# Kernel tuning notes

Hardware: AMD Instinct MI355X
Metric: run time of the kernel (lower is better)

Reference implementation:

```python
import jax, jax.numpy as jnp
import numpy as np

H_DIM = 768
N_HEADS = 12
HEAD_DIM = H_DIM // N_HEADS  # 64
LOW_RANK = 2
LR_DIM = H_DIM // LOW_RANK   # 384
SEQ = 2048
WINDOW = 1024
EOT = 50256


def _rope_tables(seq_len, dim):
    pos = jnp.arange(seq_len, dtype=jnp.float32)[:, None]
    div = jnp.exp(jnp.arange(0, dim, 2, dtype=jnp.float32) * (-np.log(10000.0) / dim))
    emb = pos * div  # (S, dim/2)
    sin = jnp.concatenate([jnp.sin(emb), jnp.sin(emb)], axis=-1)  # (S, dim)
    cos = jnp.concatenate([jnp.cos(emb), jnp.cos(emb)], axis=-1)
    return sin, cos


def _apply_rope(x, sin, cos):
    # x: (B, H, S, d); sin/cos: (S, d)
    half = x.shape[-1] // 2
    rot = jnp.concatenate([-x[..., half:], x[..., :half]], axis=-1)
    return x * cos + rot * sin


def setup_inputs() -> dict:
    key = jax.random.key(0)
    ks = jax.random.split(key, 20)
    x = jax.random.normal(ks[0], (1, SEQ, H_DIM), dtype=jnp.float32)
    # tokens with document boundaries every ~512 tokens
    tok = jax.random.randint(ks[1], (SEQ,), 0, 50257)
    tok = tok.at[::512].set(EOT)

    def lin(k, fan_in, fan_out):
        w = jax.random.normal(k, (fan_in, fan_out), dtype=jnp.float32) * 0.02
        b = jnp.zeros((fan_out,), dtype=jnp.float32)
        return w, b

    qd_w, qd_b = lin(ks[2], H_DIM, LR_DIM)
    qu_w, qu_b = lin(ks[3], LR_DIM, H_DIM)
    qr_w, qr_b = lin(ks[4], H_DIM, HEAD_DIM)
    kvd_w, kvd_b = lin(ks[5], H_DIM, LR_DIM)
    ku_w, ku_b = lin(ks[6], LR_DIM, H_DIM)
    vu_w, vu_b = lin(ks[7], LR_DIM, H_DIM * 2)
    kr_w, kr_b = lin(ks[8], H_DIM, HEAD_DIM)
    o_w, o_b = lin(ks[9], H_DIM * 2, H_DIM)
    return dict(x=x, token_seq=tok,
                qd_w=qd_w, qd_b=qd_b, qu_w=qu_w, qu_b=qu_b,
                qr_w=qr_w, qr_b=qr_b, kvd_w=kvd_w, kvd_b=kvd_b,
                ku_w=ku_w, ku_b=ku_b, vu_w=vu_w, vu_b=vu_b,
                kr_w=kr_w, kr_b=kr_b, o_w=o_w, o_b=o_b)


def _mla_forward(x, token_seq, qd_w, qd_b, qu_w, qu_b, qr_w, qr_b,
                 kvd_w, kvd_b, ku_w, ku_b, vu_w, vu_b, kr_w, kr_b, o_w, o_b):
    B, S, _ = x.shape
    sin, cos = _rope_tables(S, HEAD_DIM)
    scale = (2 * HEAD_DIM) ** (-0.5)

    # queries: low-rank down/up + shared rotary part
    q = (x @ qd_w + qd_b) @ qu_w + qu_b                     # (B,S,H_DIM)
    q = q.reshape(B, S, N_HEADS, HEAD_DIM).transpose(0, 2, 1, 3)
    qr = (x @ qr_w + qr_b)[:, None, :, :]                   # (B,1,S,hd)
    qr = jnp.broadcast_to(qr, (B, N_HEADS, S, HEAD_DIM))
    qr = _apply_rope(qr, sin, cos)
    q = jnp.concatenate([q, qr], axis=-1)                   # (B,nh,S,2hd)

    # shared low-rank kv latent
    lkv = x @ kvd_w + kvd_b                                 # (B,S,LR)
    k = (lkv @ ku_w + ku_b).reshape(B, S, N_HEADS, HEAD_DIM).transpose(0, 2, 1, 3)
    kr = (x @ kr_w + kr_b)[:, None, :, :]
    kr = jnp.broadcast_to(kr, (B, N_HEADS, S, HEAD_DIM))
    kr = _apply_rope(kr, sin, cos)
    k = jnp.concatenate([k, kr], axis=-1)                   # (B,nh,S,2hd)

    v = (lkv @ vu_w + vu_b).reshape(B, S, N_HEADS, 2 * HEAD_DIM).transpose(0, 2, 1, 3)

    # mask: causal & same-document & sliding window (<1024)
    docs = jnp.cumsum(token_seq == EOT)
    qi = jnp.arange(S)
    mask = (qi[:, None] >= qi[None, :]) \
           & (docs[:, None] == docs[None, :]) \
           & (qi[:, None] - qi[None, :] < WINDOW)           # (S,S)

    scores = jnp.einsum('bhqd,bhkd->bhqk', q, k) * scale
    scores = jnp.where(mask, scores, -jnp.inf)
    attn = jax.nn.softmax(scores, axis=-1)
    out = jnp.einsum('bhqk,bhkd->bhqd', attn, v)            # (B,nh,S,2hd)
    out = out.transpose(0, 2, 1, 3).reshape(B, S, 2 * H_DIM)
    return out @ o_w + o_b


def reference(x, token_seq, qd_w, qd_b, qu_w, qu_b, qr_w, qr_b,
              kvd_w, kvd_b, ku_w, ku_b, vu_w, vu_b, kr_w, kr_b, o_w, o_b):
    return _mla_forward(x, token_seq, qd_w, qd_b, qu_w, qu_b, qr_w, qr_b,
                        kvd_w, kvd_b, ku_w, ku_b, vu_w, vu_b, kr_w, kr_b, o_w, o_b)
```

## Files before the change

kernel.cpp:

```cpp
#include <hip/hip_runtime.h>
#include <hip/hip_bf16.h>
#include <math.h>

#define SEQ 2048
#define HDIM 768
#define NH 12
#define HD 64
#define LR 384
#define EOT 50256

typedef short s16x8 __attribute__((ext_vector_type(8)));
typedef float f32x4 __attribute__((ext_vector_type(4)));
typedef unsigned short u16x8 __attribute__((ext_vector_type(8)));
typedef unsigned short u16x4 __attribute__((ext_vector_type(4)));

__device__ __forceinline__ unsigned short f2bf(float f) {
    union { float f; unsigned u; } v; v.f = f;
    unsigned r = v.u + 0x7fffu + ((v.u >> 16) & 1u);
    return (unsigned short)(r >> 16);
}

__device__ __forceinline__ void gl_lds16(const void* g, void* l) {
    __builtin_amdgcn_global_load_lds(
        (const __attribute__((address_space(1))) unsigned int*)g,
        (__attribute__((address_space(3))) unsigned int*)l, 16, 0, 0);
}

__global__ __launch_bounds__(256)
void transpose_pack_all(const float* w0, const float* w1, const float* w2, const float* w3,
                        const float* w4, const float* w5, const float* w6, const float* w7,
                        unsigned short* t0, unsigned short* t1, unsigned short* t2, unsigned short* t3,
                        unsigned short* t4, unsigned short* t5, unsigned short* t6, unsigned short* t7,
                        const float* x, unsigned short* xb,
                        const float* qd_b, const float* kvd_b, const float* qr_b, const float* kr_b,
                        const float* qu_b, const float* ku_b, const float* vu_b,
                        float* biasA, float* biasB,
                        const int* tok, int* lastEOT) {
    __shared__ float t[64][65];
    __shared__ int smax[256];
    int b = blockIdx.x;
    const int tid = threadIdx.x;
    if (b == 1129) {
        const int base = tid * 8;
        int v[8];
        int mx = 0;
#pragma unroll
        for (int j = 0; j < 8; ++j) {
            int i = base + j;
            int f = (tok[i] == EOT) ? i : 0;
            mx = max(mx, f);
            v[j] = mx;
        }
        smax[tid] = mx;
        __syncthreads();
        for (int off = 1; off < 256; off <<= 1) {
            int val = (tid >= off) ? smax[tid - off] : 0;
            __syncthreads();
            smax[tid] = max(smax[tid], val);
            __syncthreads();
        }
        int pre = (tid > 0) ? smax[tid - 1] : 0;
#pragma unroll
        for (int j = 0; j < 8; ++j) lastEOT[base + j] = max(pre, v[j]);
        return;
    }
    if (b == 1128) {
        for (int i = tid; i < 896; i += 256) {
            float v;
            if (i < 384) v = qd_b[i];
            else if (i < 768) v = kvd_b[i - 384];
            else if (i < 832) v = qr_b[i - 768];
            else v = kr_b[i - 832];
            biasA[i] = v;
        }
        for (int i = tid; i < 3072; i += 256) {
            float v;
            if (i < 768) v = qu_b[i];
            else if (i < 1536) v = ku_b[i - 768];
            else v = vu_b[i - 1536];
            biasB[i] = v;
        }
        return;
    }
    if (b >= 744) {
        int b2 = b - 744;
        int row0 = (b2 / 12) * 64, col0 = (b2 % 12) * 64;
#pragma unroll
        for (int i = 0; i < 16; ++i) {
            int idx = tid + i * 256;
            int r = idx >> 6, c = idx & 63;
            xb[(size_t)(row0 + r) * HDIM + col0 + c] = f2bf(x[(size_t)(row0 + r) * HDIM + col0 + c]);
        }
        return;
    }
    const float* W; unsigned short* T; int K, N, lt;
    if      (b < 72)  { W = w0; T = t0; K = 768;  N = 384;  lt = b; }
    else if (b < 144) { W = w1; T = t1; K = 384;  N = 768;  lt = b - 72; }
    else if (b < 156) { W = w2; T = t2; K = 768;  N = 64;   lt = b - 144; }
    else if (b < 228) { W = w3; T = t3; K = 768;  N = 384;  lt = b - 156; }
    else if (b < 300) { W = w4; T = t4; K = 384;  N = 768;  lt = b - 228; }
    else if (b < 444) { W = w5; T = t5; K = 384;  N = 1536; lt = b - 300; }
    else if (b < 456) { W = w6; T = t6; K = 768;  N = 64;   lt = b - 444; }
    else              { W = w7; T = t7; K = 1536; N = 768;  lt = b - 456; }
    const int tn = N >> 6;
    const int n0 = (lt % tn) * 64, k0 = (lt / tn) * 64;
#pragma unroll
    for (int i = 0; i < 16; ++i) {
        int idx = tid + i * 256;
        int k = idx >> 6, n = idx & 63;
        t[k][n] = W[(size_t)(k0 + k) * N + n0 + n];
    }
    __syncthreads();
#pragma unroll
    for (int i = 0; i < 16; ++i) {
        int idx = tid + i * 256;
        int n = idx >> 6, k = idx & 63;
        T[(size_t)(n0 + n) * K + k0 + k] = f2bf(t[k][n]);
    }
}

template <int FUSE>
__global__ __launch_bounds__(256)
void gemm_mfma_kernel(const unsigned short* __restrict__ A, const unsigned short* __restrict__ Bt,
                      const float* __restrict__ bias,
                      void* __restrict__ O0, void* __restrict__ O1, void* __restrict__ O2,
                      int K, int lda) {
    __shared__ unsigned short As[2][128 * 64];
    __shared__ unsigned short Bs[2][64 * 64];
    const int tid = threadIdx.x;
    const int w = tid >> 6, lane = tid & 63, lr = lane & 15, lg = lane >> 4;
    const int row0 = blockIdx.y * 128, col0 = blockIdx.x * 64;
    const int wr = (w >> 1) * 64, wc = (w & 1) * 32;
    const unsigned short* Ab = A + ((FUSE == 2 && col0 >= 768) ? 384 : 0);

    f32x4 acc[4][2];
#pragma unroll
    for (int i = 0; i < 4; ++i)
#pragma unroll
        for (int j = 0; j < 2; ++j) acc[i][j] = f32x4{0.f, 0.f, 0.f, 0.f};

    auto stage = [&](int buf, int kt) {
#pragma unroll
        for (int i = 0; i < 4; ++i) {
            int c = tid + i * 256;
            int row = c >> 3, dgL = c & 7;
            gl_lds16(Ab + (size_t)(row0 + row) * lda + kt + (dgL ^ (row & 7)) * 8, &As[buf][c * 8]);
        }
#pragma unroll
        for (int i = 0; i < 2; ++i) {
            int c = tid + i * 256;
            int n = c >> 3, dgL = c & 7;
            gl_lds16(Bt + (size_t)(col0 + n) * K + kt + (dgL ^ (n & 7)) * 8, &Bs[buf][c * 8]);
        }
    };

    const int nkt = K >> 6;
    stage(0, 0);
    for (int t = 0; t < nkt; ++t) {
        __syncthreads();
        if (t + 1 < nkt) stage((t + 1) & 1, (t + 1) << 6);
        const unsigned short* asb = As[t & 1];
        const unsigned short* bsb = Bs[t & 1];
#pragma unroll
        for (int kk = 0; kk < 2; ++kk) {
            const int kbyte = kk * 64 + lg * 16;
#pragma unroll
            for (int mi = 0; mi < 4; ++mi) {
                const int row = wr + mi * 16 + lr;
                s16x8 a = *(const s16x8*)&asb[row * 64 + ((kbyte ^ ((row & 7) << 4)) >> 1)];
#pragma unroll
                for (int ni = 0; ni < 2; ++ni) {
                    const int n = wc + ni * 16 + lr;
                    s16x8 bfr = *(const s16x8*)&bsb[n * 64 + ((kbyte ^ ((n & 7) << 4)) >> 1)];
                    acc[mi][ni] = __builtin_amdgcn_mfma_f32_16x16x32_bf16(a, bfr, acc[mi][ni], 0, 0, 0);
                }
            }
        }
    }

    if (FUSE == 1 && col0 >= 768) {
        __syncthreads();
        float* rt = (float*)&As[0][0];
#pragma unroll
        for (int mi = 0; mi < 4; ++mi)
#pragma unroll
            for (int ni = 0; ni < 2; ++ni) {
                const int cl = wc + ni * 16 + lr;
                const float bv = bias[col0 + cl];
#pragma unroll
                for (int j = 0; j < 4; ++j)
                    rt[(wr + mi * 16 + lg * 4 + j) * 64 + cl] = acc[mi][ni][j] + bv;
            }
        __syncthreads();
        unsigned short* dst = (col0 == 768) ? (unsigned short*)O1 : (unsigned short*)O2;
        const int row = tid >> 1;
        const int i0 = (tid & 1) * 16;
        const float srow = (float)(row0 + row);
#pragma unroll
        for (int ii = 0; ii < 16; ++ii) {
            const int i = i0 + ii;
            float a = rt[row * 64 + i], b = rt[row * 64 + 32 + i];
            float div = expf((float)(2 * i) * (-logf(10000.0f) / 64.0f));
            float emb = srow * div;
            float sn, cs;
            __sincosf(emb, &sn, &cs);
            dst[(size_t)(row0 + row) * 64 + i]      = f2bf(a * cs - b * sn);
            dst[(size_t)(row0 + row) * 64 + 32 + i] = f2bf(b * cs + a * sn);
        }
        return;
    }

#pragma unroll
    for (int mi = 0; mi < 4; ++mi) {
#pragma unroll
        for (int ni = 0; ni < 2; ++ni) {
            const int col = col0 + wc + ni * 16 + lr;
            const float bv = bias[col];
            const int rbase = row0 + wr + mi * 16 + lg * 4;
            if (FUSE == 0) {
#pragma unroll
                for (int j = 0; j < 4; ++j)
                    ((float*)O0)[(size_t)(rbase + j) * HDIM + col] = acc[mi][ni][j] + bv;
            } else if (FUSE == 1) {
#pragma unroll
                for (int j = 0; j < 4; ++j)
                    ((unsigned short*)O0)[(size_t)(rbase + j) * HDIM + col] = f2bf(acc[mi][ni][j] + bv);
            } else {
                if (col < 768) {
                    const int hh = col >> 6, d = col & 63;
#pragma unroll
                    for (int j = 0; j < 4; ++j)
                        ((unsigned short*)O0)[(size_t)(rbase + j) * (NH * 64) + hh * 64 + d] = f2bf(acc[mi][ni][j] + bv);
                } else if (col < 1536) {
                    const int c2 = col - 768;
                    const int hh = c2 >> 6, d = c2 & 63;
#pragma unroll
                    for (int j = 0; j < 4; ++j)
                        ((unsigned short*)O1)[(size_t)(rbase + j) * (NH * 64) + hh * 64 + d] = f2bf(acc[mi][ni][j] + bv);
                } else {
                    const int c2 = col - 1536;
                    const int hh = c2 >> 7, d = c2 & 127;
                    u16x4 pk;
#pragma unroll
                    for (int j = 0; j < 4; ++j) pk[j] = f2bf(acc[mi][ni][j] + bv);
                    *(u16x4*)((unsigned short*)O2 + (size_t)(hh * 128 + d) * SEQ + rbase) = pk;
                }
            }
        }
    }
}

__global__ __launch_bounds__(256)
void attn_mfma_kernel(const unsigned short* __restrict__ qbuf,
                      const unsigned short* __restrict__ qrb,
                      const unsigned short* __restrict__ kbuf,
                      const unsigned short* __restrict__ krb,
                      const unsigned short* __restrict__ vbT,
                      const int* __restrict__ lastEOT,
                      unsigned short* __restrict__ aob) {
    __shared__ unsigned short Ks[2][64 * 128];
    __shared__ unsigned short Vt[2][128 * 64];
    __shared__ unsigned short Pa[4][16 * 64];

    const int h    = blockIdx.y;
    const int q0   = blockIdx.x * 64;
    const int tid  = threadIdx.x;
    const int w    = tid >> 6;
    const int lane = tid & 63;
    const int lr   = lane & 15;
    const int lg   = lane >> 4;

    const int qrow0 = q0 + w * 16 + lg * 4;
    const int qminw = q0 + w * 16;
    const int qmaxw = qminw + 15;
    const int leMinW = lastEOT[qminw];
    const int leMaxW = lastEOT[qmaxw];
    int rs[4];
#pragma unroll
    for (int r = 0; r < 4; ++r) rs[r] = lastEOT[qrow0 + r];

    s16x8 aq[4];
    {
        const int s = q0 + w * 16 + lr;
        const unsigned short* qp = qbuf + ((size_t)s * NH + h) * 64 + lg * 8;
        aq[0] = *(const s16x8*)qp;
        aq[1] = *(const s16x8*)(qp + 32);
        const unsigned short* qrp = qrb + (size_t)s * 64 + lg * 8;
        aq[2] = *(const s16x8*)qrp;
        aq[3] = *(const s16x8*)(qrp + 32);
    }

    const int kt0 = lastEOT[q0] & ~63;
    const int ntiles = (q0 + 64 - kt0) >> 6;

    float lsum[4] = {0.f, 0.f, 0.f, 0.f};
    f32x4 o[8];
#pragma unroll
    for (int n = 0; n < 8; ++n) o[n] = f32x4{0.f, 0.f, 0.f, 0.f};

    const float scale = 0.088388347648318447f;

    auto stage = [&](int buf, int k0) {
#pragma unroll
        for (int i = 0; i < 4; ++i) {
            const int c = tid + i * 256;
            const int key = c >> 4, dgL = c & 15;
            const int dg = dgL ^ (key & 7);
            const unsigned short* src = (dg < 8)
                ? kbuf + ((size_t)(k0 + key) * NH + h) * 64 + dg * 8
                : krb + (size_t)(k0 + key) * 64 + (dg - 8) * 8;
            gl_lds16(src, &Ks[buf][c * 8]);
        }
#pragma unroll
        for (int i = 0; i < 4; ++i) {
            const int c = tid + i * 256;
            const int dim = c >> 3, kgL = c & 7;
            gl_lds16(vbT + ((size_t)h * 128 + dim) * SEQ + k0 + (kgL ^ (dim & 7)) * 8, &Vt[buf][c * 8]);
        }
    };

    stage(0, kt0);
    for (int t = 0; t < ntiles; ++t) {
        const int k0 = kt0 + t * 64;
        __syncthreads();
        if (t + 1 < ntiles) stage((t + 1) & 1, k0 + 64);

        if (k0 > qmaxw || k0 + 63 < leMinW) continue;

        const unsigned short* ksb = Ks[t & 1];
        const unsigned short* vtb = Vt[t & 1];

        f32x4 s[4];
#pragma unroll
        for (int n = 0; n < 4; ++n) s[n] = f32x4{0.f, 0.f, 0.f, 0.f};
#pragma unroll
        for (int n = 0; n < 4; ++n) {
            const int key = n * 16 + lr;
            const int swz = (key & 7) << 4;
#pragma unroll
            for (int kk = 0; kk < 4; ++kk) {
                const int colb = (kk * 64 + lg * 16) ^ swz;
                s16x8 bk = *(const s16x8*)&ksb[key * 128 + (colb >> 1)];
                s[n] = __builtin_amdgcn_mfma_f32_16x16x32_bf16(aq[kk], bk, s[n], 0, 0, 0);
            }
        }

        const bool full = (k0 + 63 <= qminw) && (k0 >= leMaxW);
        float p[4][4];
        if (full) {
#pragma unroll
            for (int n = 0; n < 4; ++n)
#pragma unroll
                for (int r = 0; r < 4; ++r) {
                    float pv = __expf(s[n][r] * scale);
                    p[n][r] = pv;
                    lsum[r] += pv;
                }
        } else {
#pragma unroll
            for (int n = 0; n < 4; ++n) {
                const int k = k0 + n * 16 + lr;
#pragma unroll
                for (int r = 0; r < 4; ++r) {
                    const int qq = qrow0 + r;
                    const bool valid = (k <= qq) && (k >= rs[r]);
                    float pv = valid ? __expf(s[n][r] * scale) : 0.f;
                    p[n][r] = pv;
                    lsum[r] += pv;
                }
            }
        }

#pragma unroll
        for (int n = 0; n < 4; ++n)
#pragma unroll
            for (int r = 0; r < 4; ++r) {
                const int ql = lg * 4 + r;
                const int key = n * 16 + lr;
                const int byteoff = (key * 2) ^ ((ql & 7) << 4);
                Pa[w][ql * 64 + (byteoff >> 1)] = f2bf(p[n][r]);
            }

#pragma unroll
        for (int kk2 = 0; kk2 < 2; ++kk2) {
            const int keyb = kk2 * 32 + lg * 8;
            s16x8 ap = *(const s16x8*)&Pa[w][lr * 64 + ((((keyb * 2) ^ ((lr & 7) << 4))) >> 1)];
#pragma unroll
            for (int n = 0; n < 8; ++n) {
                const int dim = n * 16 + lr;
                s16x8 bv = *(const s16x8*)&vtb[dim * 64 + ((((keyb * 2) ^ ((dim & 7) << 4))) >> 1)];
                o[n] = __builtin_amdgcn_mfma_f32_16x16x32_bf16(ap, bv, o[n], 0, 0, 0);
            }
        }
    }

#pragma unroll
    for (int off = 1; off < 16; off <<= 1)
#pragma unroll
        for (int r = 0; r < 4; ++r) lsum[r] += __shfl_xor(lsum[r], off);

    float inv[4];
#pragma unroll
    for (int r = 0; r < 4; ++r) inv[r] = 1.f / lsum[r];
#pragma unroll
    for (int n = 0; n < 8; ++n)
#pragma unroll
        for (int r = 0; r < 4; ++r) {
            const int qq = qrow0 + r;
            aob[(size_t)qq * (2 * HDIM) + h * 128 + n * 16 + lr] = f2bf(o[n][r] * inv[r]);
        }
}

extern "C" void kernel_launch(void* const* d_in, const int* in_sizes, int n_in,
                              void* d_out, int out_size, void* d_ws, size_t ws_size,
                              hipStream_t stream) {
    (void)in_sizes; (void)n_in; (void)out_size; (void)ws_size;
    const float* x     = (const float*)d_in[0];
    const int*   tok   = (const int*)d_in[1];
    const float* qd_w  = (const float*)d_in[2];
    const float* qd_b  = (const float*)d_in[3];
    const float* qu_w  = (const float*)d_in[4];
    const float* qu_b  = (const float*)d_in[5];
    const float* qr_w  = (const float*)d_in[6];
    const float* qr_b  = (const float*)d_in[7];
    const float* kvd_w = (const float*)d_in[8];
    const float* kvd_b = (const float*)d_in[9];
    const float* ku_w  = (const float*)d_in[10];
    const float* ku_b  = (const float*)d_in[11];
    const float* vu_w  = (const float*)d_in[12];
    const float* vu_b  = (const float*)d_in[13];
    const float* kr_w  = (const float*)d_in[14];
    const float* kr_b  = (const float*)d_in[15];
    const float* o_w   = (const float*)d_in[16];
    const float* o_b   = (const float*)d_in[17];
    float* out = (float*)d_out;

    unsigned short* ws = (unsigned short*)d_ws;
    unsigned short* xb   = ws;
    unsigned short* lqkv = xb   + (size_t)SEQ * HDIM;
    unsigned short* qbuf = lqkv + (size_t)SEQ * HDIM;
    unsigned short* kbuf = qbuf + (size_t)SEQ * NH * 64;
    unsigned short* qrb  = kbuf + (size_t)SEQ * NH * 64;
    unsigned short* krb  = qrb  + (size_t)SEQ * 64;
    unsigned short* vbT  = krb  + (size_t)SEQ * 64;
    unsigned short* aob  = vbT  + (size_t)NH * 128 * SEQ;
    unsigned short* B1   = aob  + (size_t)SEQ * 2 * HDIM;
    unsigned short* B2   = B1   + (size_t)896 * HDIM;
    unsigned short* to   = B2   + (size_t)3072 * LR;
    float* biasA = (float*)(to + (size_t)HDIM * 2 * HDIM);
    float* biasB = biasA + 896;
    int* lastEOT = (int*)(biasB + 3072);

    unsigned short* tqd  = B1;
    unsigned short* tkvd = B1 + (size_t)384 * 768;
    unsigned short* tqr  = B1 + (size_t)768 * 768;
    unsigned short* tkr  = B1 + (size_t)832 * 768;
    unsigned short* tqu  = B2;
    unsigned short* tku  = B2 + (size_t)768 * 384;
    unsigned short* tvu  = B2 + (size_t)1536 * 384;

    transpose_pack_all<<<1130, 256, 0, stream>>>(qd_w, qu_w, qr_w, kvd_w, ku_w, vu_w, kr_w, o_w,
                                                 tqd, tqu, tqr, tkvd, tku, tvu, tkr, to,
                                                 x, xb, qd_b, kvd_b, qr_b, kr_b, qu_b, ku_b, vu_b,
                                                 biasA, biasB, tok, lastEOT);

    gemm_mfma_kernel<1><<<dim3(14, 16), 256, 0, stream>>>(xb, B1, biasA, lqkv, qrb, krb, HDIM, HDIM);
    gemm_mfma_kernel<2><<<dim3(48, 16), 256, 0, stream>>>(lqkv, B2, biasB, qbuf, kbuf, vbT, LR, HDIM);

    attn_mfma_kernel<<<dim3(SEQ / 64, NH), 256, 0, stream>>>(qbuf, qrb, kbuf, krb, vbT, lastEOT, aob);

    gemm_mfma_kernel<0><<<dim3(12, 16), 256, 0, stream>>>(aob, to, o_b, out, nullptr, nullptr, 2 * HDIM, 2 * HDIM);
}
```

Baseline: 81.75 us.

## Load K/V fragments directly from global memory instead of LDS staging

Drops the double-buffered LDS staging of K and V tiles and the per-tile block barrier. Each wave now reads its K/Kr and transposed-V MFMA operands straight from global memory and loops only over its own key range, set by its first row's document start. The aim is to remove barrier stalls and the work of tiles a wave skips. In exchange, the four waves each fetch the same K/V data, so global/L2 traffic rises and there is no software prefetch to hide load latency.

```diff
diff --git a/kernel.cpp b/kernel.cpp
--- a/kernel.cpp
+++ b/kernel.cpp
@@ -258,8 +258,6 @@
                       const unsigned short* __restrict__ vbT,
                       const int* __restrict__ lastEOT,
                       unsigned short* __restrict__ aob) {
-    __shared__ unsigned short Ks[2][64 * 128];
-    __shared__ unsigned short Vt[2][128 * 64];
     __shared__ unsigned short Pa[4][16 * 64];
 
     const int h    = blockIdx.y;
@@ -290,8 +288,8 @@
         aq[3] = *(const s16x8*)(qrp + 32);
     }
 
-    const int kt0 = lastEOT[q0] & ~63;
-    const int ntiles = (q0 + 64 - kt0) >> 6;
+    const int kt0 = leMinW & ~63;
+    const int ntiles = (qmaxw >> 6) - (kt0 >> 6) + 1;
 
     float lsum[4] = {0.f, 0.f, 0.f, 0.f};
     f32x4 o[8];
@@ -300,49 +298,24 @@
 
     const float scale = 0.088388347648318447f;
 
-    auto stage = [&](int buf, int k0) {
-#pragma unroll
-        for (int i = 0; i < 4; ++i) {
-            const int c = tid + i * 256;
-            const int key = c >> 4, dgL = c & 15;
-            const int dg = dgL ^ (key & 7);
-            const unsigned short* src = (dg < 8)
-                ? kbuf + ((size_t)(k0 + key) * NH + h) * 64 + dg * 8
-                : krb + (size_t)(k0 + key) * 64 + (dg - 8) * 8;
-            gl_lds16(src, &Ks[buf][c * 8]);
-        }
-#pragma unroll
-        for (int i = 0; i < 4; ++i) {
-            const int c = tid + i * 256;
-            const int dim = c >> 3, kgL = c & 7;
-            gl_lds16(vbT + ((size_t)h * 128 + dim) * SEQ + k0 + (kgL ^ (dim & 7)) * 8, &Vt[buf][c * 8]);
-        }
-    };
-
-    stage(0, kt0);
+    const unsigned short* kb_h = kbuf + (size_t)h * 64;
+    const unsigned short* v_h  = vbT + (size_t)h * 128 * SEQ;
+
     for (int t = 0; t < ntiles; ++t) {
         const int k0 = kt0 + t * 64;
-        __syncthreads();
-        if (t + 1 < ntiles) stage((t + 1) & 1, k0 + 64);
-
-        if (k0 > qmaxw || k0 + 63 < leMinW) continue;
-
-        const unsigned short* ksb = Ks[t & 1];
-        const unsigned short* vtb = Vt[t & 1];
 
         f32x4 s[4];
 #pragma unroll
         for (int n = 0; n < 4; ++n) s[n] = f32x4{0.f, 0.f, 0.f, 0.f};
 #pragma unroll
         for (int n = 0; n < 4; ++n) {
-            const int key = n * 16 + lr;
-            const int swz = (key & 7) << 4;
-#pragma unroll
-            for (int kk = 0; kk < 4; ++kk) {
-                const int colb = (kk * 64 + lg * 16) ^ swz;
-                s16x8 bk = *(const s16x8*)&ksb[key * 128 + (colb >> 1)];
-                s[n] = __builtin_amdgcn_mfma_f32_16x16x32_bf16(aq[kk], bk, s[n], 0, 0, 0);
-            }
+            const int key = k0 + n * 16 + lr;
+            const unsigned short* kp  = kb_h + (size_t)key * (NH * 64) + lg * 8;
+            const unsigned short* krp = krb + (size_t)key * 64 + lg * 8;
+            s[n] = __builtin_amdgcn_mfma_f32_16x16x32_bf16(aq[0], *(const s16x8*)kp, s[n], 0, 0, 0);
+            s[n] = __builtin_amdgcn_mfma_f32_16x16x32_bf16(aq[1], *(const s16x8*)(kp + 32), s[n], 0, 0, 0);
+            s[n] = __builtin_amdgcn_mfma_f32_16x16x32_bf16(aq[2], *(const s16x8*)krp, s[n], 0, 0, 0);
+            s[n] = __builtin_amdgcn_mfma_f32_16x16x32_bf16(aq[3], *(const s16x8*)(krp + 32), s[n], 0, 0, 0);
         }
 
         const bool full = (k0 + 63 <= qminw) && (k0 >= leMaxW);
@@ -388,7 +361,7 @@
 #pragma unroll
             for (int n = 0; n < 8; ++n) {
                 const int dim = n * 16 + lr;
-                s16x8 bv = *(const s16x8*)&vtb[dim * 64 + ((((keyb * 2) ^ ((dim & 7) << 4))) >> 1)];
+                s16x8 bv = *(const s16x8*)(v_h + (size_t)dim * SEQ + k0 + keyb);
                 o[n] = __builtin_amdgcn_mfma_f32_16x16x32_bf16(ap, bv, o[n], 0, 0, 0);
             }
         }
```

After: 129.2 us. 58.1% more time.
